# Kernel tuning notes

Measured on AMD Instinct MI355X. Metric: run time of the kernel, lower is better.

The kernel has to match this reference:

```python
import jax, jax.numpy as jnp
import numpy as np

B, S, H, NH, NL = 8, 768, 768, 12, 5
HD = H // NH


def setup_inputs() -> dict:
    key = jax.random.key(0)
    ks = jax.random.split(key, 14)
    lim = 1.0 / np.sqrt(H)
    u = lambda k, shape: jax.random.uniform(k, shape, jnp.float32, -lim, lim)
    inp = {}
    inp["hidden_states"] = jax.random.normal(ks[0], (B, S, H), jnp.float32)
    inp["language_ids"] = jax.random.randint(ks[1], (B,), 0, NL)
    inp["attention_mask"] = jnp.ones((B, S), jnp.int32)
    # per-language query/key Linear weights (torch Linear: y = x @ W.T + b)
    inp["Wq_lang"] = u(ks[2], (NL, H, H))
    inp["bq_lang"] = u(ks[3], (NL, H))
    inp["Wk_lang"] = u(ks[4], (NL, H, H))
    inp["bk_lang"] = u(ks[5], (NL, H))
    # nn.MultiheadAttention params
    inp["in_proj_w"] = u(ks[6], (3 * H, H))
    inp["in_proj_b"] = u(ks[7], (3 * H,))
    inp["out_proj_w"] = u(ks[8], (H, H))
    inp["out_proj_b"] = u(ks[9], (H,))
    # alignment matrices: initialized as eye in torch; perturb so products are non-trivial
    inp["align"] = jnp.eye(H, dtype=jnp.float32) + 0.02 * jax.random.normal(ks[10], (NL, NL, H, H), jnp.float32)
    # output projection + layer norm
    inp["proj_w"] = u(ks[11], (H, H))
    inp["proj_b"] = u(ks[12], (H,))
    inp["ln_g"] = jnp.ones((H,), jnp.float32)
    inp["ln_b"] = jnp.zeros((H,), jnp.float32)
    return inp


def reference(hidden_states, language_ids, attention_mask, Wq_lang, bq_lang, Wk_lang, bk_lang,
              in_proj_w, in_proj_b, out_proj_w, out_proj_b, align, proj_w, proj_b, ln_g, ln_b):
    b, s, h = hidden_states.shape
    lang = language_ids
    # language-routed query/key transforms (grouped GEMM via gather of per-lang weights)
    q = jnp.einsum('bsi,boi->bso', hidden_states, Wq_lang[lang]) + bq_lang[lang][:, None, :]
    k = jnp.einsum('bsi,boi->bso', hidden_states, Wk_lang[lang]) + bk_lang[lang][:, None, :]
    # nn.MultiheadAttention (eval mode, no dropout). Note: the torch module's
    # key_padding_mask is always all-False due to a masked_fill(-inf).bool() bug,
    # so no masking is applied -- reproduced faithfully here.
    wq, wk, wv = jnp.split(in_proj_w, 3, axis=0)
    bq_, bk_, bv_ = jnp.split(in_proj_b, 3)
    Q = (jnp.einsum('bsi,oi->bso', q, wq) + bq_).reshape(b, s, NH, HD)
    K = (jnp.einsum('bsi,oi->bso', k, wk) + bk_).reshape(b, s, NH, HD)
    V = (jnp.einsum('bsi,oi->bso', hidden_states, wv) + bv_).reshape(b, s, NH, HD)
    scores = jnp.einsum('bqhd,bkhd->bhqk', Q, K) / np.sqrt(HD).astype(np.float32)
    attn = jax.nn.softmax(scores, axis=-1)  # [b, nh, s, s]
    ctx = jnp.einsum('bhqk,bkhd->bqhd', attn, V).reshape(b, s, h)
    aligned = jnp.einsum('bsi,oi->bso', ctx, out_proj_w) + out_proj_b
    # pairwise alignment chain: for each i, aligned_i @ prod_{j: lang_j != lang_i} A[lang_i, lang_j]
    # (i==j skipped; same-language pairs skipped since no A exists)
    same = lang[:, None] == lang[None, :]  # [b, b]; diagonal is True -> identity
    sel = align[lang[:, None], lang[None, :]]  # [b, b, h, h]
    I = jnp.eye(h, dtype=hidden_states.dtype)
    Smat = jnp.where(same[:, :, None, None], I, sel)  # [b(i), b(j), h, h]
    def step(carry, Sj):  # carry [b,h,h], Sj [b,h,h] for one j across all i
        return carry @ Sj, None
    M, _ = jax.lax.scan(step, jnp.tile(I, (b, 1, 1)), jnp.swapaxes(Smat, 0, 1))
    aligned = jnp.einsum('bsh,bhk->bsk', aligned, M)
    # output projection + residual layer norm
    out = jnp.einsum('bsi,oi->bso', aligned, proj_w) + proj_b
    x = out + hidden_states
    mu = x.mean(-1, keepdims=True)
    var = x.var(-1, keepdims=True)
    return (x - mu) / jnp.sqrt(var + 1e-5) * ln_g + ln_b
```

## Files before the change

kernel.cpp:

```cpp
#include <hip/hip_runtime.h>

#define Bn 8
#define Sn 768
#define Hn 768
#define NHn 12
#define HDn 64
#define NLn 5

typedef unsigned short u16;
typedef __bf16 bf16x8 __attribute__((ext_vector_type(8)));
typedef short s16x8 __attribute__((ext_vector_type(8)));
typedef float f32x4 __attribute__((ext_vector_type(4)));
typedef unsigned short u16x4 __attribute__((ext_vector_type(4)));

static __device__ __forceinline__ float bf2f(u16 v) {
    return __uint_as_float(((unsigned)v) << 16);
}
static __device__ __forceinline__ u16 f2bf(float f) {
    unsigned u = __float_as_uint(f);
    unsigned r = u + 0x7fffu + ((u >> 16) & 1u);
    return (u16)(r >> 16);
}
static __device__ __forceinline__ bf16x8 ld8(const u16* p) {
    return *reinterpret_cast<const bf16x8*>(p);
}
static __device__ __forceinline__ void glds16(const u16* g, u16* l) {
    __builtin_amdgcn_global_load_lds(
        (const __attribute__((address_space(1))) void*)g,
        (__attribute__((address_space(3))) void*)l, 16, 0, 0);
}

#define PREP_NF2B 6912
#define PREP_NTR  1584
__global__ __launch_bounds__(256) void k_prep(
    const float* __restrict__ hidden, u16* __restrict__ hb,
    const float* __restrict__ ipw, u16* __restrict__ ipwb,
    const float* __restrict__ projw, u16* __restrict__ pjwb,
    const float* __restrict__ Wq, const float* __restrict__ Wk,
    const float* __restrict__ opw, u16* __restrict__ S, u16* __restrict__ opwT,
    const float* __restrict__ ipb,
    const float* __restrict__ bq_lang, const float* __restrict__ bk_lang,
    float* __restrict__ beff)
{
    __shared__ float T[64][65];
    const size_t HH = (size_t)Hn * Hn;
    const int bid = blockIdx.x, tid = threadIdx.x;
    if (bid < PREP_NF2B) {
        const int n0 = (int)(Bn * Sn * Hn / 4), n1 = (int)(3 * HH / 4), n2 = (int)(HH / 4);
        int i = bid * 256 + tid;
        const float* s; u16* d; int off;
        if (i < n0)                { s = hidden; d = hb;   off = i; }
        else if (i < n0 + n1)      { s = ipw;    d = ipwb; off = i - n0; }
        else if (i < n0 + n1 + n2) { s = projw;  d = pjwb; off = i - n0 - n1; }
        else return;
        float4 v = reinterpret_cast<const float4*>(s)[off];
        u16x4 o;
        o[0] = f2bf(v.x); o[1] = f2bf(v.y); o[2] = f2bf(v.z); o[3] = f2bf(v.w);
        reinterpret_cast<u16x4*>(d)[off] = o;
    } else if (bid < PREP_NF2B + PREP_NTR) {
        int b2 = bid - PREP_NF2B;
        int z = b2 / 144, r = b2 % 144;
        int bx = r % 12, by = r / 12;
        const float* src;
        u16* dst;
        if (z < 5)       { src = Wq + (size_t)z * HH;       dst = S + (size_t)z * HH; }
        else if (z < 10) { src = Wk + (size_t)(z - 5) * HH; dst = S + (size_t)z * HH; }
        else             { src = opw;                        dst = opwT; }
        int i0 = bx * 64, o0 = by * 64;
        int x = tid & 63, ys = tid >> 6;
        for (int rr = ys; rr < 64; rr += 4)
            T[rr][x] = src[(size_t)(o0 + rr) * Hn + i0 + x];
        __syncthreads();
        for (int rr = ys; rr < 64; rr += 4)
            dst[(size_t)(i0 + rr) * Hn + o0 + x] = f2bf(T[x][rr]);
    } else {
        int b3 = bid - PREP_NF2B - PREP_NTR;
        int ox = b3 % 3, y = b3 / 3;
        int o = ox * 256 + tid;
        int which = y / 5, l = y % 5;
        const float4* w = reinterpret_cast<const float4*>(ipw + (size_t)which * HH + (size_t)o * Hn);
        const float4* bv = reinterpret_cast<const float4*>(((which ? bk_lang : bq_lang) + (size_t)l * Hn));
        float s = 0.f;
        for (int j = 0; j < Hn / 4; ++j) {
            float4 a = w[j], b = bv[j];
            s += a.x * b.x + a.y * b.y + a.z * b.z + a.w * b.w;
        }
        s += ipb[which * Hn + o];
        beff[(size_t)(which * 5 + l) * Hn + o] = s;
    }
}

template<int TM>
__device__ __forceinline__ void gemm_core(
    const u16* __restrict__ A, int lda,
    const u16* __restrict__ Bw, int ldb,
    const float* __restrict__ bias,
    const float* __restrict__ addres,
    u16* __restrict__ outH, float* __restrict__ outF,
    u16* __restrict__ outVT, int ldc,
    int m0, int n0, float scale)
{
    constexpr int MI = TM / 32;
    constexpr int AIT = TM / 64;
    __shared__ u16 As[3 * TM * 32];
    __shared__ u16 Bs[3 * 128 * 32];
    const int tid = threadIdx.x;
    const int lane = tid & 63, wave = tid >> 6;
    const int lrow = lane & 15, lquad = lane >> 4;
    const int wm = (wave >> 1) * (TM / 2), wn = (wave & 1) * 64;

    const u16* gA = A + (size_t)(m0 + (tid >> 2)) * lda + (tid & 3) * 8;
    const u16* gB = Bw + (size_t)(n0 + (tid >> 2)) * ldb + (tid & 3) * 8;

    f32x4 z = {0.f, 0.f, 0.f, 0.f};
    f32x4 acc[MI][4];
    #pragma unroll
    for (int i = 0; i < MI; ++i)
        #pragma unroll
        for (int j = 0; j < 4; ++j) acc[i][j] = z;

    auto stage = [&](int bs, int k0) {
        #pragma unroll
        for (int it = 0; it < AIT; ++it)
            glds16(gA + (size_t)(it * 64) * lda + k0, &As[bs * TM * 32 + (tid + 256 * it) * 8]);
        #pragma unroll
        for (int it = 0; it < 2; ++it)
            glds16(gB + (size_t)(it * 64) * ldb + k0, &Bs[bs * 128 * 32 + (tid + 256 * it) * 8]);
    };
    auto compute = [&](int bc) {
        const u16* Ab = &As[bc * TM * 32];
        const u16* Bb = &Bs[bc * 128 * 32];
        bf16x8 af[MI], bf_[4];
        #pragma unroll
        for (int i = 0; i < MI; ++i)
            af[i] = ld8(&Ab[(wm + i * 16 + lrow) * 32 + lquad * 8]);
        #pragma unroll
        for (int j = 0; j < 4; ++j)
            bf_[j] = ld8(&Bb[(wn + j * 16 + lrow) * 32 + lquad * 8]);
        #pragma unroll
        for (int i = 0; i < MI; ++i)
            #pragma unroll
            for (int j = 0; j < 4; ++j)
                acc[i][j] = __builtin_amdgcn_mfma_f32_16x16x32_bf16(af[i], bf_[j], acc[i][j], 0, 0, 0);
    };

    stage(0, 0);
    stage(1, 32);
    int bc = 0, bs = 2;
    for (int kt = 0; kt < 24; ++kt) {
        if (kt < 23) {
            if constexpr (TM == 256) {
                asm volatile("s_waitcnt vmcnt(6)" ::: "memory");
            } else {
                asm volatile("s_waitcnt vmcnt(4)" ::: "memory");
            }
        } else {
            asm volatile("s_waitcnt vmcnt(0)" ::: "memory");
        }
        __builtin_amdgcn_s_barrier();
        if (kt < 22) {
            stage(bs, (kt + 2) * 32);
            bs = (bs == 2) ? 0 : bs + 1;
        }
        compute(bc);
        bc = (bc == 2) ? 0 : bc + 1;
    }

    #pragma unroll
    for (int i = 0; i < MI; ++i) {
        #pragma unroll
        for (int j = 0; j < 4; ++j) {
            int col = n0 + wn + j * 16 + lrow;
            float bv = bias ? bias[col] : 0.f;
            if (outVT) {
                int row0 = m0 + wm + i * 16 + lquad * 4;
                int bb = row0 / Sn, s = row0 % Sn;
                int hh = col >> 6, dd = col & 63;
                u16x4 o;
                #pragma unroll
                for (int r = 0; r < 4; ++r) o[r] = f2bf((acc[i][j][r] + bv) * scale);
                *reinterpret_cast<u16x4*>(
                    outVT + (((size_t)bb * NHn + hh) * 64 + dd) * Sn + s) = o;
            } else {
                #pragma unroll
                for (int r = 0; r < 4; ++r) {
                    int row = m0 + wm + i * 16 + lquad * 4 + r;
                    float v = (acc[i][j][r] + bv) * scale;
                    if (addres) v += addres[(size_t)row * ldc + col];
                    if (outF) outF[(size_t)row * ldc + col] = v;
                    else      outH[(size_t)row * ldc + col] = f2bf(v);
                }
            }
        }
    }
}

__device__ __forceinline__ void gemm64(
    const u16* __restrict__ A, const u16* __restrict__ Bw,
    const float* __restrict__ bias, const float* __restrict__ addres,
    u16* __restrict__ outH, float* __restrict__ outF,
    int m0, int n0)
{
    __shared__ u16 As[3 * 64 * 32];
    __shared__ u16 Bs[3 * 64 * 32];
    const int tid = threadIdx.x;
    const int lane = tid & 63, wave = tid >> 6;
    const int lrow = lane & 15, lquad = lane >> 4;
    const int wm = (wave >> 1) * 32, wn = (wave & 1) * 32;

    const u16* gA = A + (size_t)(m0 + (tid >> 2)) * Hn + (tid & 3) * 8;
    const u16* gB = Bw + (size_t)(n0 + (tid >> 2)) * Hn + (tid & 3) * 8;

    f32x4 z = {0.f, 0.f, 0.f, 0.f};
    f32x4 acc[2][2];
    #pragma unroll
    for (int i = 0; i < 2; ++i)
        #pragma unroll
        for (int j = 0; j < 2; ++j) acc[i][j] = z;

    auto stage = [&](int bs, int k0) {
        glds16(gA + k0, &As[bs * 64 * 32 + tid * 8]);
        glds16(gB + k0, &Bs[bs * 64 * 32 + tid * 8]);
    };
    auto compute = [&](int bc) {
        const u16* Ab = &As[bc * 64 * 32];
        const u16* Bb = &Bs[bc * 64 * 32];
        bf16x8 af[2], bf_[2];
        #pragma unroll
        for (int i = 0; i < 2; ++i)
            af[i] = ld8(&Ab[(wm + i * 16 + lrow) * 32 + lquad * 8]);
        #pragma unroll
        for (int j = 0; j < 2; ++j)
            bf_[j] = ld8(&Bb[(wn + j * 16 + lrow) * 32 + lquad * 8]);
        #pragma unroll
        for (int i = 0; i < 2; ++i)
            #pragma unroll
            for (int j = 0; j < 2; ++j)
                acc[i][j] = __builtin_amdgcn_mfma_f32_16x16x32_bf16(af[i], bf_[j], acc[i][j], 0, 0, 0);
    };

    stage(0, 0);
    stage(1, 32);
    int bc = 0, bs = 2;
    for (int kt = 0; kt < 24; ++kt) {
        if (kt < 23) {
            asm volatile("s_waitcnt vmcnt(2)" ::: "memory");
        } else {
            asm volatile("s_waitcnt vmcnt(0)" ::: "memory");
        }
        __builtin_amdgcn_s_barrier();
        if (kt < 22) {
            stage(bs, (kt + 2) * 32);
            bs = (bs == 2) ? 0 : bs + 1;
        }
        compute(bc);
        bc = (bc == 2) ? 0 : bc + 1;
    }

    #pragma unroll
    for (int i = 0; i < 2; ++i)
        #pragma unroll
        for (int j = 0; j < 2; ++j) {
            int col = n0 + wn + j * 16 + lrow;
            float bv = bias ? bias[col] : 0.f;
            #pragma unroll
            for (int r = 0; r < 4; ++r) {
                int row_ = m0 + wm + i * 16 + lquad * 4 + r;
                float v = acc[i][j][r] + bv;
                if (addres) v += addres[(size_t)row_ * Hn + col];
                if (outF) outF[(size_t)row_ * Hn + col] = v;
                else      outH[(size_t)row_ * Hn + col] = f2bf(v);
            }
        }
}


__global__ __launch_bounds__(256) void k_gemm_qkv(
    const u16* __restrict__ A,
    const u16* __restrict__ Sq, const u16* __restrict__ Sk,
    const u16* __restrict__ Wv,
    const float* __restrict__ beff, const float* __restrict__ ipb,
    const int* __restrict__ lang,
    u16* __restrict__ outQ, u16* __restrict__ outK, u16* __restrict__ outVT)
{
    const size_t HH = (size_t)Hn * Hn;
    int z = blockIdx.z;
    int m0 = blockIdx.x * 128, n0 = blockIdx.y * 128;
    int l = lang[blockIdx.x / 6];
    if (z == 0) {
        gemm_core<128>(A, Hn, Sq + (size_t)l * HH, Hn, beff + (size_t)l * Hn,
                       nullptr, outQ, nullptr, nullptr, Hn, m0, n0, 0.125f);
    } else if (z == 1) {
        gemm_core<128>(A, Hn, Sk + (size_t)l * HH, Hn, beff + (size_t)(5 + l) * Hn,
                       nullptr, outK, nullptr, nullptr, Hn, m0, n0, 1.f);
    } else {
        gemm_core<128>(A, Hn, Wv, Hn, ipb + 2 * Hn,
                       nullptr, nullptr, nullptr, outVT, Hn, m0, n0, 1.f);
    }
}

__global__ __launch_bounds__(256) void k_comb10(
    const u16* __restrict__ ipwb, u16* __restrict__ S)
{
    const size_t HH = (size_t)Hn * Hn;
    int z = blockIdx.z;
    const u16* Aop = ipwb + (z < 5 ? 0 : HH);
    gemm64(Aop, S + (size_t)z * HH, nullptr, nullptr,
           S + (size_t)(10 + z) * HH, nullptr,
           blockIdx.x * 64, blockIdx.y * 64);
}

__global__ __launch_bounds__(256) void k_chain_first(
    const u16* __restrict__ alignb, const int* __restrict__ lang,
    u16* __restrict__ out5)
{
    const size_t HH = (size_t)Hn * Hn;
    int l = blockIdx.z, lj = lang[Bn - 1];
    u16* dst = out5 + (size_t)l * HH;
    int i0 = blockIdx.x * 64, o0 = blockIdx.y * 64;
    const int tid = threadIdx.x;
    if (lj == l) {
        #pragma unroll
        for (int it = 0; it < 2; ++it) {
            int s = tid + 256 * it;
            int ri = s >> 3, c8 = s & 7;
            s16x8 v;
            #pragma unroll
            for (int e = 0; e < 8; ++e)
                v[e] = (short)((i0 + ri == o0 + c8 * 8 + e) ? 0x3F80 : 0);
            *reinterpret_cast<s16x8*>(dst + (size_t)(i0 + ri) * Hn + o0 + c8 * 8) = v;
        }
    } else {
        const u16* src = alignb + ((size_t)l * NLn + lj) * HH;
        __shared__ u16 T[64][72];
        #pragma unroll
        for (int it = 0; it < 2; ++it) {
            int s = tid + 256 * it;
            int r = s >> 3, c8 = s & 7;
            s16x8 v = *reinterpret_cast<const s16x8*>(
                src + (size_t)(o0 + r) * Hn + i0 + c8 * 8);
            #pragma unroll
            for (int e = 0; e < 8; ++e) T[c8 * 8 + e][r] = (u16)v[e];
        }
        __syncthreads();
        #pragma unroll
        for (int it = 0; it < 2; ++it) {
            int s = tid + 256 * it;
            int ri = s >> 3, c8 = s & 7;
            s16x8 v = *reinterpret_cast<const s16x8*>(&T[ri][c8 * 8]);
            *reinterpret_cast<s16x8*>(dst + (size_t)(i0 + ri) * Hn + o0 + c8 * 8) = v;
        }
    }
}

__global__ __launch_bounds__(256) void k_chain64(
    u16* __restrict__ rC, u16* __restrict__ rD,
    const u16* __restrict__ alignb, const int* __restrict__ lang, int j)
{
    const size_t HH = (size_t)Hn * Hn;
    int l = blockIdx.z;
    int lj = lang[j];
    if (lj == l) return;
    int c = 0;
    for (int jj = j + 1; jj <= 6; ++jj) c += (lang[jj] != l) ? 1 : 0;
    const u16* in = ((c & 1) ? rD : rC) + (size_t)l * HH;
    u16* out = ((c & 1) ? rC : rD) + (size_t)l * HH;
    const u16* F = alignb + ((size_t)l * NLn + lj) * HH;
    gemm64(in, F, nullptr, nullptr, out, nullptr,
           blockIdx.x * 64, blockIdx.y * 64);
}

__global__ __launch_bounds__(256) void k_uop(
    const u16* __restrict__ opwT,
    const u16* __restrict__ rC, const u16* __restrict__ rD,
    const int* __restrict__ lang, const float* __restrict__ opb,
    u16* __restrict__ U5, float* __restrict__ opbeff)
{
    const size_t HH = (size_t)Hn * Hn;
    int bid = blockIdx.x;
    int l = (bid < 720) ? (bid / 144) : ((bid - 720) / 3);
    int pf = 0;
    for (int jj = 0; jj <= 6; ++jj) pf += (lang[jj] != l) ? 1 : 0;
    const u16* MT = ((pf & 1) ? rD : rC) + (size_t)l * HH;
    if (bid < 720) {
        int r = bid % 144;
        gemm64(opwT, MT, nullptr, nullptr, U5 + (size_t)l * HH, nullptr,
               (r % 12) * 64, (r / 12) * 64);
    } else {
        int b2 = bid - 720;
        int n = (b2 % 3) * 256 + threadIdx.x;
        const u16* mt = MT + (size_t)n * Hn;
        float s = 0.f;
        for (int k = 0; k < Hn; k += 8) {
            s16x8 v = *reinterpret_cast<const s16x8*>(mt + k);
            #pragma unroll
            for (int jq = 0; jq < 8; ++jq) s += opb[k + jq] * bf2f((u16)v[jq]);
        }
        opbeff[(size_t)l * Hn + n] = s;
    }
}

__global__ __launch_bounds__(256) void k_wb2(
    const u16* __restrict__ pjwb, const u16* __restrict__ U5,
    const float* __restrict__ opbeff, const float* __restrict__ projw,
    const float* __restrict__ projb,
    u16* __restrict__ W5, float* __restrict__ bias2)
{
    const size_t HH = (size_t)Hn * Hn;
    int bid = blockIdx.x;
    if (bid < 720) {
        int z = bid / 144, r = bid % 144;
        gemm64(pjwb, U5 + (size_t)z * HH, nullptr, nullptr,
               W5 + (size_t)z * HH, nullptr,
               (r % 12) * 64, (r / 12) * 64);
    } else {
        int b2 = bid - 720;
        int m = (b2 % 3) * 256 + threadIdx.x;
        int l = b2 / 3;
        const float4* w = reinterpret_cast<const float4*>(projw + (size_t)m * Hn);
        const float4* ob = reinterpret_cast<const float4*>(opbeff + (size_t)l * Hn);
        float s = 0.f;
        for (int jq = 0; jq < Hn / 4; ++jq) {
            float4 a = w[jq], b = ob[jq];
            s += a.x * b.x + a.y * b.y + a.z * b.z + a.w * b.w;
        }
        bias2[(size_t)l * Hn + m] = s + projb[m];
    }
}

__global__ __launch_bounds__(256) void k_xfused(
    const u16* __restrict__ ctx, const u16* __restrict__ W5,
    const float* __restrict__ bias2, const int* __restrict__ lang,
    const float* __restrict__ hidden, float* __restrict__ x)
{
    int l = lang[blockIdx.x / 12];
    gemm64(ctx, W5 + (size_t)l * Hn * Hn, bias2 + (size_t)l * Hn,
           hidden, nullptr, x,
           blockIdx.x * 64, blockIdx.y * 64);
}

__global__ __launch_bounds__(512) void k_attn_conv(
    const u16* __restrict__ Q, const u16* __restrict__ K,
    const u16* __restrict__ VT, u16* __restrict__ ctx,
    const float* __restrict__ alignf, u16* __restrict__ alignb)
{
    __shared__ u16 Ks[2][64 * 64];
    __shared__ u16 Vs[2][64 * 64];
    __shared__ u16 Pw[8][16 * 72];

    const int bid = blockIdx.x, tid = threadIdx.x;
    if (bid >= 576) {
        int base = (bid - 576) * 4096 + tid;
        #pragma unroll
        for (int it = 0; it < 8; ++it) {
            int i = base + it * 512;
            float4 v = reinterpret_cast<const float4*>(alignf)[i];
            u16x4 o;
            o[0] = f2bf(v.x); o[1] = f2bf(v.y); o[2] = f2bf(v.z); o[3] = f2bf(v.w);
            reinterpret_cast<u16x4*>(alignb)[i] = o;
        }
        return;
    }

    const int q0 = (bid % 6) * 128, h = (bid / 6) % NHn, bz = bid / 72;
    const int wave = tid >> 6, lane = tid & 63;
    const int lrow = lane & 15, lquad = lane >> 4;
    const int sw = lrow & 7;

    const u16* Qp = Q + ((size_t)(bz * Sn + q0 + wave * 16 + lrow)) * Hn + h * HDn;
    const u16* Kb = K + (size_t)bz * Sn * Hn + h * HDn;
    const u16* Vb = VT + ((size_t)(bz * NHn + h) * 64) * Sn;

    bf16x8 qa0 = ld8(Qp + lquad * 8);
    bf16x8 qa1 = ld8(Qp + 32 + lquad * 8);

    f32x4 z4 = {0.f, 0.f, 0.f, 0.f};
    float m_r[4], l_l[4];
    f32x4 oacc[4];
    #pragma unroll
    for (int r = 0; r < 4; ++r) { m_r[r] = -1e30f; l_l[r] = 0.f; }
    #pragma unroll
    for (int jd = 0; jd < 4; ++jd) oacc[jd] = z4;

    const int krow = tid >> 3, kp = (tid & 7) ^ (krow & 7);
    const u16* kg = Kb + (size_t)krow * Hn + kp * 8;
    const u16* vg = Vb + (size_t)krow * Sn + kp * 8;

    auto stage = [&](int bs, int t0) {
        glds16(kg + (size_t)t0 * Hn, &Ks[bs][tid * 8]);
        glds16(vg + t0, &Vs[bs][tid * 8]);
    };

    auto compute = [&](int bc) {
        f32x4 sc[4];
        __builtin_amdgcn_s_setprio(1);
        #pragma unroll
        for (int j = 0; j < 4; ++j) {
            int base = (j * 16 + lrow) * 64 + ((lquad ^ sw) * 8);
            f32x4 s = __builtin_amdgcn_mfma_f32_16x16x32_bf16(qa0, ld8(&Ks[bc][base]), z4, 0, 0, 0);
            sc[j] = __builtin_amdgcn_mfma_f32_16x16x32_bf16(qa1, ld8(&Ks[bc][base ^ 32]), s, 0, 0, 0);
        }
        __builtin_amdgcn_s_setprio(0);
        float tmax[4];
        #pragma unroll
        for (int r = 0; r < 4; ++r)
            tmax[r] = fmaxf(fmaxf(sc[0][r], sc[1][r]), fmaxf(sc[2][r], sc[3][r]));
        #pragma unroll
        for (int off = 1; off < 16; off <<= 1)
            #pragma unroll
            for (int r = 0; r < 4; ++r)
                tmax[r] = fmaxf(tmax[r], __shfl_xor(tmax[r], off));
        bool grow = (tmax[0] > m_r[0] + 8.f) | (tmax[1] > m_r[1] + 8.f) |
                    (tmax[2] > m_r[2] + 8.f) | (tmax[3] > m_r[3] + 8.f);
        if (grow) {
            #pragma unroll
            for (int r = 0; r < 4; ++r) {
                float mn = fmaxf(m_r[r], tmax[r]);
                float a = __expf(m_r[r] - mn);
                m_r[r] = mn;
                l_l[r] *= a;
                #pragma unroll
                for (int jd = 0; jd < 4; ++jd) oacc[jd][r] *= a;
            }
        }
        float ps[4] = {0.f, 0.f, 0.f, 0.f};
        #pragma unroll
        for (int j = 0; j < 4; ++j)
            #pragma unroll
            for (int r = 0; r < 4; ++r) {
                float p = __expf(sc[j][r] - m_r[r]);
                ps[r] += p;
                Pw[wave][(lquad * 4 + r) * 72 + j * 16 + lrow] = f2bf(p);
            }
        #pragma unroll
        for (int r = 0; r < 4; ++r) l_l[r] += ps[r];
        bf16x8 pa0 = ld8(&Pw[wave][lrow * 72 + lquad * 8]);
        bf16x8 pa1 = ld8(&Pw[wave][lrow * 72 + 32 + lquad * 8]);
        __builtin_amdgcn_s_setprio(1);
        #pragma unroll
        for (int jd = 0; jd < 4; ++jd) {
            int vbase = (jd * 16 + lrow) * 64 + ((lquad ^ sw) * 8);
            oacc[jd] = __builtin_amdgcn_mfma_f32_16x16x32_bf16(pa0, ld8(&Vs[bc][vbase]), oacc[jd], 0, 0, 0);
            oacc[jd] = __builtin_amdgcn_mfma_f32_16x16x32_bf16(pa1, ld8(&Vs[bc][vbase ^ 32]), oacc[jd], 0, 0, 0);
        }
        __builtin_amdgcn_s_setprio(0);
    };

    stage(0, 0);
    stage(1, 64);
    for (int kt = 0; kt < 12; ++kt) {
        if (kt < 11) {
            asm volatile("s_waitcnt vmcnt(2)" ::: "memory");
        } else {
            asm volatile("s_waitcnt vmcnt(0)" ::: "memory");
        }
        __builtin_amdgcn_s_barrier();
        compute(kt & 1);
        if (kt < 10) {
            __builtin_amdgcn_s_barrier();
            stage(kt & 1, (kt + 2) * 64);
        }
    }

    #pragma unroll
    for (int off = 1; off < 16; off <<= 1)
        #pragma unroll
        for (int r = 0; r < 4; ++r)
            l_l[r] += __shfl_xor(l_l[r], off);

    float rl[4];
    #pragma unroll
    for (int r = 0; r < 4; ++r) rl[r] = 1.f / l_l[r];
    #pragma unroll
    for (int jd = 0; jd < 4; ++jd)
        #pragma unroll
        for (int r = 0; r < 4; ++r) {
            size_t row = (size_t)bz * Sn + q0 + wave * 16 + lquad * 4 + r;
            ctx[row * Hn + h * HDn + jd * 16 + lrow] = f2bf(oacc[jd][r] * rl[r]);
        }
}

__global__ __launch_bounds__(64) void k_ln(
    float* x, const float* __restrict__ g, const float* __restrict__ beta)
{
    size_t row = blockIdx.x;
    float* xr = x + row * Hn;
    int lane = threadIdx.x;
    float v[12];
    float s = 0.f, ss = 0.f;
    #pragma unroll
    for (int i = 0; i < 12; ++i) {
        v[i] = xr[lane + i * 64];
        s += v[i];
        ss += v[i] * v[i];
    }
    #pragma unroll
    for (int off = 1; off < 64; off <<= 1) {
        s  += __shfl_xor(s, off);
        ss += __shfl_xor(ss, off);
    }
    float mu = s * (1.f / Hn);
    float var = ss * (1.f / Hn) - mu * mu;
    float inv = rsqrtf(var + 1e-5f);
    #pragma unroll
    for (int i = 0; i < 12; ++i) {
        int c = lane + i * 64;
        xr[c] = (v[i] - mu) * inv * g[c] + beta[c];
    }
}

extern "C" void kernel_launch(void* const* d_in, const int* in_sizes, int n_in,
                              void* d_out, int out_size, void* d_ws, size_t ws_size,
                              hipStream_t stream)
{
    (void)in_sizes; (void)n_in; (void)out_size; (void)ws_size;

    const float* hidden  = (const float*)d_in[0];
    const int*   lang    = (const int*)d_in[1];
    const float* Wq_lang = (const float*)d_in[3];
    const float* bq_lang = (const float*)d_in[4];
    const float* Wk_lang = (const float*)d_in[5];
    const float* bk_lang = (const float*)d_in[6];
    const float* ipw     = (const float*)d_in[7];
    const float* ipb     = (const float*)d_in[8];
    const float* opw     = (const float*)d_in[9];
    const float* opb     = (const float*)d_in[10];
    const float* align   = (const float*)d_in[11];
    const float* projw   = (const float*)d_in[12];
    const float* projb   = (const float*)d_in[13];
    const float* ln_g    = (const float*)d_in[14];
    const float* ln_b    = (const float*)d_in[15];
    float* out = (float*)d_out;

    const size_t HH  = (size_t)Hn * Hn;
    const size_t BSH = (size_t)Bn * Sn * Hn;
    const size_t AHH = (size_t)NLn * NLn * HH;

    u16* rA = (u16*)d_ws;
    u16* rB = rA + BSH;
    u16* rC = rB + BSH;
    u16* rD = rC + BSH;
    u16* ipwb = rD + BSH;
    u16* pjwb = ipwb + 3 * HH;
    u16* opwT = pjwb + HH;
    u16* alignb = opwT + HH;
    float* beff   = (float*)(alignb + AHH);
    float* opbeff = beff + 10 * Hn;
    float* bias2  = opbeff + 5 * Hn;

    u16* S = alignb;

    k_prep<<<(unsigned)(PREP_NF2B + PREP_NTR + 30), 256, 0, stream>>>(
        hidden, rA, ipw, ipwb, projw, pjwb,
        Wq_lang, Wk_lang, opw, S, opwT,
        ipb, bq_lang, bk_lang, beff);

    k_comb10<<<dim3(12, 12, 10), 256, 0, stream>>>(ipwb, S);

    k_gemm_qkv<<<dim3(48, 6, 3), 256, 0, stream>>>(
        rA, S + 10 * HH, S + 15 * HH, ipwb + 2 * HH, beff, ipb, lang, rB, rC, rD);

    k_attn_conv<<<1476, 512, 0, stream>>>(rB, rC, rD, rA, align, alignb);

    k_chain_first<<<dim3(12, 12, NLn), 256, 0, stream>>>(alignb, lang, rC);
    for (int j = Bn - 2; j >= 0; --j)
        k_chain64<<<dim3(12, 12, NLn), 256, 0, stream>>>(rC, rD, alignb, lang, j);

    k_uop<<<735, 256, 0, stream>>>(opwT, rC, rD, lang, opb, rB, opbeff);
    k_wb2<<<735, 256, 0, stream>>>(pjwb, rB, opbeff, projw, projb, rC, bias2);

    k_xfused<<<dim3(96, 12), 256, 0, stream>>>(rA, rC, bias2, lang, hidden, out);
    k_ln<<<(unsigned)(Bn * Sn), 64, 0, stream>>>(out, ln_g, ln_b);
}
```

Baseline: 483.0 us.

## Replace sequential alignment chain with log-depth tree reduction of matrix products

The per-language chain of seven dependent 768x768 matrix products becomes a three-level binary tree. Pairs are multiplied in parallel, then pairs of pairs, using a transposed bf16 copy of the alignment matrices so that both operand orientations are available. The align conversion now writes both a normal and a transposed bf16 copy, and the buffers are remapped. This cuts the number of serial kernel launches and exposes more parallel blocks per launch, at the cost of extra conversion and transpose traffic and more workspace.

```diff
diff --git a/kernel.cpp b/kernel.cpp
--- a/kernel.cpp
+++ b/kernel.cpp
@@ -196,13 +196,12 @@
 }
 
 __device__ __forceinline__ void gemm64(
+    u16* As, u16* Bs,
     const u16* __restrict__ A, const u16* __restrict__ Bw,
     const float* __restrict__ bias, const float* __restrict__ addres,
     u16* __restrict__ outH, float* __restrict__ outF,
     int m0, int n0)
 {
-    __shared__ u16 As[3 * 64 * 32];
-    __shared__ u16 Bs[3 * 64 * 32];
     const int tid = threadIdx.x;
     const int lane = tid & 63, wave = tid >> 6;
     const int lrow = lane & 15, lquad = lane >> 4;
@@ -272,6 +271,54 @@
                 else      outH[(size_t)row_ * Hn + col] = f2bf(v);
             }
         }
+}
+
+static __device__ __forceinline__ void ident64(u16* dst, int m0, int n0)
+{
+    const int tid = threadIdx.x;
+    #pragma unroll
+    for (int it = 0; it < 2; ++it) {
+        int s = tid + 256 * it;
+        int ri = s >> 3, c8 = s & 7;
+        s16x8 v;
+        #pragma unroll
+        for (int e = 0; e < 8; ++e)
+            v[e] = (short)((m0 + ri == n0 + c8 * 8 + e) ? 0x3F80 : 0);
+        *reinterpret_cast<s16x8*>(dst + (size_t)(m0 + ri) * Hn + n0 + c8 * 8) = v;
+    }
+}
+static __device__ __forceinline__ void copy64(u16* dst, const u16* src, int m0, int n0)
+{
+    const int tid = threadIdx.x;
+    #pragma unroll
+    for (int it = 0; it < 2; ++it) {
+        int s = tid + 256 * it;
+        int row = s >> 3, seg = s & 7;
+        *reinterpret_cast<s16x8*>(dst + (size_t)(m0 + row) * Hn + n0 + seg * 8) =
+            *reinterpret_cast<const s16x8*>(src + (size_t)(m0 + row) * Hn + n0 + seg * 8);
+    }
+}
+static __device__ __forceinline__ void tcopy64(u16* dst, const u16* src, int m0, int n0, u16* lds)
+{
+    u16 (*T)[72] = reinterpret_cast<u16(*)[72]>(lds);
+    const int tid = threadIdx.x;
+    #pragma unroll
+    for (int it = 0; it < 2; ++it) {
+        int s = tid + 256 * it;
+        int rr = s >> 3, c8 = s & 7;
+        s16x8 v = *reinterpret_cast<const s16x8*>(
+            src + (size_t)(n0 + rr) * Hn + m0 + c8 * 8);
+        #pragma unroll
+        for (int e = 0; e < 8; ++e) T[c8 * 8 + e][rr] = (u16)v[e];
+    }
+    __syncthreads();
+    #pragma unroll
+    for (int it = 0; it < 2; ++it) {
+        int s = tid + 256 * it;
+        int ri = s >> 3, c8 = s & 7;
+        *reinterpret_cast<s16x8*>(dst + (size_t)(m0 + ri) * Hn + n0 + c8 * 8) =
+            *reinterpret_cast<const s16x8*>(&T[ri][c8 * 8]);
+    }
 }
 
 
@@ -302,94 +349,119 @@
 __global__ __launch_bounds__(256) void k_comb10(
     const u16* __restrict__ ipwb, u16* __restrict__ S)
 {
+    __shared__ u16 As[3 * 64 * 32];
+    __shared__ u16 Bs[3 * 64 * 32];
     const size_t HH = (size_t)Hn * Hn;
     int z = blockIdx.z;
     const u16* Aop = ipwb + (z < 5 ? 0 : HH);
-    gemm64(Aop, S + (size_t)z * HH, nullptr, nullptr,
+    gemm64(As, Bs, Aop, S + (size_t)z * HH, nullptr, nullptr,
            S + (size_t)(10 + z) * HH, nullptr,
            blockIdx.x * 64, blockIdx.y * 64);
 }
 
-__global__ __launch_bounds__(256) void k_chain_first(
-    const u16* __restrict__ alignb, const int* __restrict__ lang,
-    u16* __restrict__ out5)
-{
-    const size_t HH = (size_t)Hn * Hn;
-    int l = blockIdx.z, lj = lang[Bn - 1];
-    u16* dst = out5 + (size_t)l * HH;
-    int i0 = blockIdx.x * 64, o0 = blockIdx.y * 64;
-    const int tid = threadIdx.x;
-    if (lj == l) {
-        #pragma unroll
-        for (int it = 0; it < 2; ++it) {
-            int s = tid + 256 * it;
-            int ri = s >> 3, c8 = s & 7;
-            s16x8 v;
-            #pragma unroll
-            for (int e = 0; e < 8; ++e)
-                v[e] = (short)((i0 + ri == o0 + c8 * 8 + e) ? 0x3F80 : 0);
-            *reinterpret_cast<s16x8*>(dst + (size_t)(i0 + ri) * Hn + o0 + c8 * 8) = v;
-        }
+
+__global__ __launch_bounds__(256) void k_chainL1(
+    const u16* __restrict__ alignb, const u16* __restrict__ alignbT,
+    const int* __restrict__ lang, u16* __restrict__ N1)
+{
+    __shared__ u16 As[3 * 64 * 32];
+    __shared__ u16 Bs[3 * 64 * 32];
+    const size_t HH = (size_t)Hn * Hn;
+    int idx = blockIdx.z, l = idx >> 2, node = idx & 3;
+    int ja = 7 - node * 2, jb = 6 - node * 2;
+    bool tr = node & 1;
+    int la = lang[ja], lb = lang[jb];
+    bool sa = (la == l), sb = (lb == l);
+    u16* dst = N1 + (size_t)idx * HH;
+    int m0 = blockIdx.x * 64, n0 = blockIdx.y * 64;
+    if (sa && sb) {
+        ident64(dst, m0, n0);
+    } else if (sa) {
+        copy64(dst, (tr ? alignb : alignbT) + ((size_t)l * NLn + lb) * HH, m0, n0);
+    } else if (sb) {
+        copy64(dst, (tr ? alignb : alignbT) + ((size_t)l * NLn + la) * HH, m0, n0);
+    } else if (!tr) {
+        gemm64(As, Bs, alignbT + ((size_t)l * NLn + la) * HH,
+               alignb + ((size_t)l * NLn + lb) * HH,
+               nullptr, nullptr, dst, nullptr, m0, n0);
     } else {
-        const u16* src = alignb + ((size_t)l * NLn + lj) * HH;
-        __shared__ u16 T[64][72];
-        #pragma unroll
-        for (int it = 0; it < 2; ++it) {
-            int s = tid + 256 * it;
-            int r = s >> 3, c8 = s & 7;
-            s16x8 v = *reinterpret_cast<const s16x8*>(
-                src + (size_t)(o0 + r) * Hn + i0 + c8 * 8);
-            #pragma unroll
-            for (int e = 0; e < 8; ++e) T[c8 * 8 + e][r] = (u16)v[e];
-        }
-        __syncthreads();
-        #pragma unroll
-        for (int it = 0; it < 2; ++it) {
-            int s = tid + 256 * it;
-            int ri = s >> 3, c8 = s & 7;
-            s16x8 v = *reinterpret_cast<const s16x8*>(&T[ri][c8 * 8]);
-            *reinterpret_cast<s16x8*>(dst + (size_t)(i0 + ri) * Hn + o0 + c8 * 8) = v;
-        }
-    }
-}
-
-__global__ __launch_bounds__(256) void k_chain64(
-    u16* __restrict__ rC, u16* __restrict__ rD,
-    const u16* __restrict__ alignb, const int* __restrict__ lang, int j)
-{
+        gemm64(As, Bs, alignb + ((size_t)l * NLn + lb) * HH,
+               alignbT + ((size_t)l * NLn + la) * HH,
+               nullptr, nullptr, dst, nullptr, m0, n0);
+    }
+}
+
+__global__ __launch_bounds__(256) void k_chainL2(
+    const u16* __restrict__ N1, const int* __restrict__ lang,
+    u16* __restrict__ Q2)
+{
+    __shared__ u16 As[3 * 64 * 32];
+    __shared__ u16 Bs[3 * 64 * 32];
+    const size_t HH = (size_t)Hn * Hn;
+    int idx = blockIdx.z, l = idx >> 1, q = idx & 1;
+    int m0 = blockIdx.x * 64, n0 = blockIdx.y * 64;
+    const u16* Pa  = N1 + (size_t)(l * 4 + 0) * HH;
+    const u16* PbT = N1 + (size_t)(l * 4 + 1) * HH;
+    const u16* Pc  = N1 + (size_t)(l * 4 + 2) * HH;
+    const u16* PdT = N1 + (size_t)(l * 4 + 3) * HH;
+    if (q == 0) {
+        u16* dst = Q2 + (size_t)l * HH;
+        bool ia = (lang[7] == l) && (lang[6] == l);
+        bool ib = (lang[5] == l) && (lang[4] == l);
+        if (ia && ib)      ident64(dst, m0, n0);
+        else if (ia)       tcopy64(dst, PbT, m0, n0, As);
+        else if (ib)       copy64(dst, Pa, m0, n0);
+        else               gemm64(As, Bs, Pa, PbT, nullptr, nullptr, dst, nullptr, m0, n0);
+    } else {
+        u16* dst = Q2 + (size_t)(5 + l) * HH;
+        bool ic = (lang[3] == l) && (lang[2] == l);
+        bool id = (lang[1] == l) && (lang[0] == l);
+        if (ic && id)      ident64(dst, m0, n0);
+        else if (ic)       copy64(dst, PdT, m0, n0);
+        else if (id)       tcopy64(dst, Pc, m0, n0, As);
+        else               gemm64(As, Bs, PdT, Pc, nullptr, nullptr, dst, nullptr, m0, n0);
+    }
+}
+
+__global__ __launch_bounds__(256) void k_chainL3(
+    const u16* __restrict__ Q2, const int* __restrict__ lang,
+    u16* __restrict__ MT)
+{
+    __shared__ u16 As[3 * 64 * 32];
+    __shared__ u16 Bs[3 * 64 * 32];
     const size_t HH = (size_t)Hn * Hn;
     int l = blockIdx.z;
-    int lj = lang[j];
-    if (lj == l) return;
-    int c = 0;
-    for (int jj = j + 1; jj <= 6; ++jj) c += (lang[jj] != l) ? 1 : 0;
-    const u16* in = ((c & 1) ? rD : rC) + (size_t)l * HH;
-    u16* out = ((c & 1) ? rC : rD) + (size_t)l * HH;
-    const u16* F = alignb + ((size_t)l * NLn + lj) * HH;
-    gemm64(in, F, nullptr, nullptr, out, nullptr,
-           blockIdx.x * 64, blockIdx.y * 64);
+    int m0 = blockIdx.x * 64, n0 = blockIdx.y * 64;
+    const u16* Qa  = Q2 + (size_t)l * HH;
+    const u16* QbT = Q2 + (size_t)(5 + l) * HH;
+    u16* dst = MT + (size_t)l * HH;
+    bool iA = (lang[7] == l) && (lang[6] == l) && (lang[5] == l) && (lang[4] == l);
+    bool iB = (lang[3] == l) && (lang[2] == l) && (lang[1] == l) && (lang[0] == l);
+    if (iA && iB)      ident64(dst, m0, n0);
+    else if (iA)       tcopy64(dst, QbT, m0, n0, As);
+    else if (iB)       copy64(dst, Qa, m0, n0);
+    else               gemm64(As, Bs, Qa, QbT, nullptr, nullptr, dst, nullptr, m0, n0);
 }
 
 __global__ __launch_bounds__(256) void k_uop(
-    const u16* __restrict__ opwT,
-    const u16* __restrict__ rC, const u16* __restrict__ rD,
-    const int* __restrict__ lang, const float* __restrict__ opb,
+    const u16* __restrict__ opwT, const u16* __restrict__ MT,
+    const float* __restrict__ opb,
     u16* __restrict__ U5, float* __restrict__ opbeff)
 {
+    __shared__ u16 As[3 * 64 * 32];
+    __shared__ u16 Bs[3 * 64 * 32];
     const size_t HH = (size_t)Hn * Hn;
     int bid = blockIdx.x;
-    int l = (bid < 720) ? (bid / 144) : ((bid - 720) / 3);
-    int pf = 0;
-    for (int jj = 0; jj <= 6; ++jj) pf += (lang[jj] != l) ? 1 : 0;
-    const u16* MT = ((pf & 1) ? rD : rC) + (size_t)l * HH;
     if (bid < 720) {
-        int r = bid % 144;
-        gemm64(opwT, MT, nullptr, nullptr, U5 + (size_t)l * HH, nullptr,
+        int z = bid / 144, r = bid % 144;
+        gemm64(As, Bs, opwT, MT + (size_t)z * HH, nullptr, nullptr,
+               U5 + (size_t)z * HH, nullptr,
                (r % 12) * 64, (r / 12) * 64);
     } else {
         int b2 = bid - 720;
         int n = (b2 % 3) * 256 + threadIdx.x;
-        const u16* mt = MT + (size_t)n * Hn;
+        int l = b2 / 3;
+        const u16* mt = MT + ((size_t)l * Hn + n) * Hn;
         float s = 0.f;
         for (int k = 0; k < Hn; k += 8) {
             s16x8 v = *reinterpret_cast<const s16x8*>(mt + k);
@@ -406,11 +478,13 @@
     const float* __restrict__ projb,
     u16* __restrict__ W5, float* __restrict__ bias2)
 {
+    __shared__ u16 As[3 * 64 * 32];
+    __shared__ u16 Bs[3 * 64 * 32];
     const size_t HH = (size_t)Hn * Hn;
     int bid = blockIdx.x;
     if (bid < 720) {
         int z = bid / 144, r = bid % 144;
-        gemm64(pjwb, U5 + (size_t)z * HH, nullptr, nullptr,
+        gemm64(As, Bs, pjwb, U5 + (size_t)z * HH, nullptr, nullptr,
                W5 + (size_t)z * HH, nullptr,
                (r % 12) * 64, (r / 12) * 64);
     } else {
@@ -433,8 +507,10 @@
     const float* __restrict__ bias2, const int* __restrict__ lang,
     const float* __restrict__ hidden, float* __restrict__ x)
 {
+    __shared__ u16 As[3 * 64 * 32];
+    __shared__ u16 Bs[3 * 64 * 32];
     int l = lang[blockIdx.x / 12];
-    gemm64(ctx, W5 + (size_t)l * Hn * Hn, bias2 + (size_t)l * Hn,
+    gemm64(As, Bs, ctx, W5 + (size_t)l * Hn * Hn, bias2 + (size_t)l * Hn,
            hidden, nullptr, x,
            blockIdx.x * 64, blockIdx.y * 64);
 }
@@ -442,23 +518,30 @@
 __global__ __launch_bounds__(512) void k_attn_conv(
     const u16* __restrict__ Q, const u16* __restrict__ K,
     const u16* __restrict__ VT, u16* __restrict__ ctx,
-    const float* __restrict__ alignf, u16* __restrict__ alignb)
+    const float* __restrict__ alignf, u16* __restrict__ alignb,
+    u16* __restrict__ alignbT)
 {
     __shared__ u16 Ks[2][64 * 64];
     __shared__ u16 Vs[2][64 * 64];
     __shared__ u16 Pw[8][16 * 72];
 
     const int bid = blockIdx.x, tid = threadIdx.x;
+    const size_t HH = (size_t)Hn * Hn;
     if (bid >= 576) {
-        int base = (bid - 576) * 4096 + tid;
-        #pragma unroll
-        for (int it = 0; it < 8; ++it) {
-            int i = base + it * 512;
-            float4 v = reinterpret_cast<const float4*>(alignf)[i];
-            u16x4 o;
-            o[0] = f2bf(v.x); o[1] = f2bf(v.y); o[2] = f2bf(v.z); o[3] = f2bf(v.w);
-            reinterpret_cast<u16x4*>(alignb)[i] = o;
-        }
+        int t = bid - 576;
+        int mat = t / 144, r = t % 144;
+        int i0 = (r % 12) * 64, o0 = (r / 12) * 64;
+        const float* src = alignf + (size_t)mat * HH;
+        float (*T)[65] = reinterpret_cast<float(*)[65]>(&Pw[0][0]);
+        int x = tid & 63, ys = tid >> 6;
+        for (int rr = ys; rr < 64; rr += 8) {
+            float v = src[(size_t)(o0 + rr) * Hn + i0 + x];
+            alignb[(size_t)mat * HH + (size_t)(o0 + rr) * Hn + i0 + x] = f2bf(v);
+            T[rr][x] = v;
+        }
+        __syncthreads();
+        for (int rr = ys; rr < 64; rr += 8)
+            alignbT[(size_t)mat * HH + (size_t)(i0 + rr) * Hn + o0 + x] = f2bf(T[x][rr]);
         return;
     }
 
@@ -644,11 +727,17 @@
     u16* pjwb = ipwb + 3 * HH;
     u16* opwT = pjwb + HH;
     u16* alignb = opwT + HH;
-    float* beff   = (float*)(alignb + AHH);
+    u16* alignbT = alignb + AHH;
+    float* beff   = (float*)(alignbT + AHH);
     float* opbeff = beff + 10 * Hn;
     float* bias2  = opbeff + 5 * Hn;
 
     u16* S = alignb;
+    u16* N1 = rB;
+    u16* Q2 = alignbT;
+    u16* MT = alignb;
+    u16* U5 = alignb + 5 * HH;
+    u16* W5 = alignb + 10 * HH;
 
     k_prep<<<(unsigned)(PREP_NF2B + PREP_NTR + 30), 256, 0, stream>>>(
         hidden, rA, ipw, ipwb, projw, pjwb,
@@ -660,15 +749,15 @@
     k_gemm_qkv<<<dim3(48, 6, 3), 256, 0, stream>>>(
         rA, S + 10 * HH, S + 15 * HH, ipwb + 2 * HH, beff, ipb, lang, rB, rC, rD);
 
-    k_attn_conv<<<1476, 512, 0, stream>>>(rB, rC, rD, rA, align, alignb);
-
-    k_chain_first<<<dim3(12, 12, NLn), 256, 0, stream>>>(alignb, lang, rC);
-    for (int j = Bn - 2; j >= 0; --j)
-        k_chain64<<<dim3(12, 12, NLn), 256, 0, stream>>>(rC, rD, alignb, lang, j);
-
-    k_uop<<<735, 256, 0, stream>>>(opwT, rC, rD, lang, opb, rB, opbeff);
-    k_wb2<<<735, 256, 0, stream>>>(pjwb, rB, opbeff, projw, projb, rC, bias2);
-
-    k_xfused<<<dim3(96, 12), 256, 0, stream>>>(rA, rC, bias2, lang, hidden, out);
+    k_attn_conv<<<576 + 3600, 512, 0, stream>>>(rB, rC, rD, rA, align, alignb, alignbT);
+
+    k_chainL1<<<dim3(12, 12, 20), 256, 0, stream>>>(alignb, alignbT, lang, N1);
+    k_chainL2<<<dim3(12, 12, 10), 256, 0, stream>>>(N1, lang, Q2);
+    k_chainL3<<<dim3(12, 12, 5), 256, 0, stream>>>(Q2, lang, MT);
+
+    k_uop<<<735, 256, 0, stream>>>(opwT, MT, opb, U5, opbeff);
+    k_wb2<<<735, 256, 0, stream>>>(pjwb, U5, opbeff, projw, projb, W5, bias2);
+
+    k_xfused<<<dim3(96, 12), 256, 0, stream>>>(rA, W5, bias2, lang, hidden, out);
     k_ln<<<(unsigned)(Bn * Sn), 64, 0, stream>>>(out, ln_g, ln_b);
 }
```

Result: faster. 469.8 us (-2.7%).
